# Performance work log

Measured on AMD Instinct MI355X. Metric: run time of the kernel, lower is better.

## Reference

```python
import jax, jax.numpy as jnp
import numpy as np

EPS = 1e-5

def rmsnorm(x, g):
    var = jnp.mean(jnp.square(x), axis=-1, keepdims=True)
    return x * jax.lax.rsqrt(var + EPS) * g

def setup_inputs() -> dict:
    key = jax.random.key(0)
    ks = jax.random.split(key, 8)
    B, S, T, D = 2, 2048, 2048, 1024
    H, HKV, HD = 16, 4, 64
    std = 0.02
    return {
        "x": jax.random.normal(ks[0], (B, S, D), jnp.float32),
        "kv": jax.random.normal(ks[1], (B, T, D), jnp.float32),
        "wq": jax.random.normal(ks[2], (H * HD, D), jnp.float32) * std,
        "wk": jax.random.normal(ks[3], (HKV * HD, D), jnp.float32) * std,
        "wv": jax.random.normal(ks[4], (HKV * HD, D), jnp.float32) * std,
        "wo": jax.random.normal(ks[5], (D, H * HD), jnp.float32) * std,
        "gq": jnp.ones((D,), jnp.float32),
        "gkv": jnp.ones((D,), jnp.float32),
    }

def reference(x, kv, wq, wk, wv, wo, gq, gkv):
    B, S, D = x.shape
    T = kv.shape[1]
    H, HKV, HD = 16, 4, 64
    R = H // HKV  # heads per kv group
    xn = rmsnorm(x, gq)
    kvn = rmsnorm(kv, gkv)
    # projections
    q = (xn @ wq.T).reshape(B, S, HKV, R, HD)   # grouped query heads
    k = (kvn @ wk.T).reshape(B, T, HKV, HD)
    v = (kvn @ wv.T).reshape(B, T, HKV, HD)
    scale = 1.0 / jnp.sqrt(jnp.float32(HD))
    # block-mask is None -> full dense cross attention; GQA via broadcast einsum
    scores = jnp.einsum('bsgrd,btgd->bgrst', q, k) * scale  # [B,HKV,R,S,T]
    probs = jax.nn.softmax(scores, axis=-1)
    out = jnp.einsum('bgrst,btgd->bsgrd', probs, v)  # [B,S,HKV,R,HD]
    out = out.reshape(B, S, H * HD) @ wo.T
    return x + out
```

## Files before the change

kernel.cpp:

```cpp
#include <hip/hip_runtime.h>

#define DEV __device__ __forceinline__

typedef __attribute__((ext_vector_type(8))) _Float16 h8;
typedef __attribute__((ext_vector_type(4))) float f32x4;
typedef __attribute__((ext_vector_type(16))) float f32x16;
typedef __fp16 __attribute__((ext_vector_type(2))) hh2;

DEV unsigned short f2h(float f) {
  union { _Float16 h[2]; unsigned short u[2]; } v;
  v.h[0] = (_Float16)f;
  return v.u[0];
}

DEV float h2f(unsigned short u) {
  union { _Float16 h[2]; unsigned short u[2]; } v;
  v.u[0] = u;
  return (float)v.h[0];
}

DEV void async_load16(const void* g, void* l) {
  __builtin_amdgcn_global_load_lds(
      (const __attribute__((address_space(1))) void*)g,
      (__attribute__((address_space(3))) void*)l,
      16, 0, 0);
}

DEV void pl32swap(unsigned int& a, unsigned int& b) {
  asm("v_permlane32_swap_b32 %0, %1" : "+v"(a), "+v"(b));
}


__global__ __launch_bounds__(256) void prep(const float* __restrict__ x,
                                            const float* __restrict__ kv,
                                            const float* __restrict__ wq,
                                            const float* __restrict__ wk,
                                            const float* __restrict__ wv,
                                            const float* __restrict__ wo,
                                            const float* __restrict__ gq,
                                            const float* __restrict__ gkv,
                                            unsigned short* __restrict__ wqb,
                                            unsigned short* __restrict__ wkvb,
                                            unsigned short* __restrict__ wob,
                                            unsigned short* __restrict__ xn,
                                            unsigned short* __restrict__ kvn,
                                            float qscale) {
  const int b = blockIdx.x, tid = threadIdx.x;
  if (b < 2560) {
    const float* src;
    unsigned short* dst;
    float sc = 1.0f;
    int base;
    if (b < 1024) { src = wq; dst = wqb; sc = qscale; base = b; }
    else if (b < 1280) { src = wk; dst = wkvb; base = b - 1024; }
    else if (b < 1536) { src = wv; dst = wkvb + 262144; base = b - 1280; }
    else { src = wo; dst = wob; base = b - 1536; }
    const int i = (base * 256 + tid) * 4;
    float4 v = *(const float4*)&src[i];
    ushort4 o;
    o.x = f2h(v.x * sc); o.y = f2h(v.y * sc);
    o.z = f2h(v.z * sc); o.w = f2h(v.w * sc);
    *(ushort4*)&dst[i] = o;
    return;
  }
  int row = b - 2560;
  const float* src;
  const float* g;
  unsigned short* dst;
  if (row < 4096) { src = x; g = gq; dst = xn; }
  else { row -= 4096; src = kv; g = gkv; dst = kvn; }
  const float* xr = src + (size_t)row * 1024;
  float4 v = *(const float4*)&xr[tid * 4];
  float ss = v.x * v.x + v.y * v.y + v.z * v.z + v.w * v.w;
  ss += __shfl_xor(ss, 32); ss += __shfl_xor(ss, 16);
  ss += __shfl_xor(ss, 8);  ss += __shfl_xor(ss, 4);
  ss += __shfl_xor(ss, 2);  ss += __shfl_xor(ss, 1);
  __shared__ float red[4];
  if ((tid & 63) == 0) red[tid >> 6] = ss;
  __syncthreads();
  float tot = red[0] + red[1] + red[2] + red[3];
  float inv = rsqrtf(tot * (1.0f / 1024.0f) + 1e-5f);
  float4 gv = *(const float4*)&g[tid * 4];
  ushort4 o;
  o.x = f2h(v.x * inv * gv.x); o.y = f2h(v.y * inv * gv.y);
  o.z = f2h(v.z * inv * gv.z); o.w = f2h(v.w * inv * gv.w);
  *(ushort4*)&dst[(size_t)row * 1024 + tid * 4] = o;
}

__global__ __launch_bounds__(256) void proj_gemm(const unsigned short* __restrict__ xn,
                                                 const unsigned short* __restrict__ kvn,
                                                 const unsigned short* __restrict__ wqb,
                                                 const unsigned short* __restrict__ wkvb,
                                                 unsigned short* __restrict__ qb,
                                                 unsigned short* __restrict__ kb,
                                                 unsigned short* __restrict__ vTb) {
  __shared__ unsigned short Al[2][2][128 * 32];
  __shared__ unsigned short Bl[2][2][64 * 32];
  const int tid = threadIdx.x;
  const int w = tid >> 6, l = tid & 63;
  const int quad = l >> 4, ln = l & 15;
  const int wm0 = (w >> 1) * 64, wn0 = (w & 1) * 32;
  const int r4 = l >> 2;
  const int c4s = (((l & 3) ^ ((l >> 3) & 3))) * 8;
  const int qs8 = (quad ^ ((l >> 1) & 3)) * 8;

  int z = blockIdx.x;
  const unsigned short *A, *W;
  int m0, n0, isq;
  if (z < 512) {
    A = xn; W = wqb; isq = 1;
    m0 = (((z >> 7) << 3) + (z & 7)) * 128;
    n0 = ((z >> 3) & 15) * 64;
  } else {
    z -= 512; A = kvn; W = wkvb; isq = 0;
    m0 = (((z >> 6) << 3) + (z & 7)) * 128;
    n0 = ((z >> 3) & 7) * 64;
  }

  f32x4 acc[4][2] = {};

  auto stage = [&](int buf, int kk) {
#pragma unroll
    for (int j = 0; j < 6; ++j) {
      const int idx = w * 6 + j;
      if (idx < 16) {
        const int p = idx >> 3, rb = (idx & 7) * 16;
        async_load16(A + (size_t)(m0 + rb + r4) * 1024 + kk + p * 32 + c4s,
                     &Al[buf][p][rb * 32]);
      } else {
        const int ib = idx - 16;
        const int p = ib >> 2, rb = (ib & 3) * 16;
        async_load16(W + (size_t)(n0 + rb + r4) * 1024 + kk + p * 32 + c4s,
                     &Bl[buf][p][rb * 32]);
      }
    }
  };

  stage(0, 0);
#pragma unroll 2
  for (int it = 0; it < 16; ++it) {
    const int buf = it & 1;
    __syncthreads();
    if (it < 15) stage(buf ^ 1, (it + 1) * 64);
#pragma unroll
    for (int kc = 0; kc < 2; ++kc) {
      h8 af[4], bf[2];
#pragma unroll
      for (int mi = 0; mi < 4; ++mi)
        af[mi] = *(const h8*)&Al[buf][kc][(wm0 + mi * 16 + ln) * 32 + qs8];
#pragma unroll
      for (int ni = 0; ni < 2; ++ni)
        bf[ni] = *(const h8*)&Bl[buf][kc][(wn0 + ni * 16 + ln) * 32 + qs8];
#pragma unroll
      for (int mi = 0; mi < 4; ++mi)
#pragma unroll
        for (int ni = 0; ni < 2; ++ni)
          acc[mi][ni] = __builtin_amdgcn_mfma_f32_16x16x32_f16(af[mi], bf[ni], acc[mi][ni], 0, 0, 0);
    }
  }

#pragma unroll
  for (int mi = 0; mi < 4; ++mi)
#pragma unroll
    for (int ni = 0; ni < 2; ++ni)
#pragma unroll
      for (int r = 0; r < 4; ++r) {
        const int row = m0 + wm0 + mi * 16 + quad * 4 + r;
        const int col = n0 + wn0 + ni * 16 + ln;
        const unsigned short v = f2h(acc[mi][ni][r]);
        if (isq) {
          qb[((size_t)row << 10) + col] = v;
        } else if (col < 256) {
          kb[(size_t)row * 256 + col] = v;
        } else {
          const int c2 = col - 256, gg = c2 >> 6, dd = c2 & 63;
          const int bb = row >> 11, t = row & 2047;
          vTb[((size_t)((bb * 4 + gg) * 64 + dd) << 11) + t] = v;
        }
      }
}

__global__ __launch_bounds__(256) void o_gemm(const unsigned short* __restrict__ O0,
                                              const unsigned short* __restrict__ O1,
                                              const float* __restrict__ l0p,
                                              const float* __restrict__ l1p,
                                              const unsigned short* __restrict__ wob,
                                              const float* __restrict__ x,
                                              float* __restrict__ out) {
  __shared__ unsigned short Al[2][2][128 * 32];
  __shared__ unsigned short Bl[2][2][64 * 32];
  __shared__ float Linv[16 * 128];
  const int tid = threadIdx.x;
  const int w = tid >> 6, l = tid & 63;
  const int quad = l >> 4, ln = l & 15;
  const int wm0 = (w >> 1) * 64, wn0 = (w & 1) * 32;
  const int r4 = l >> 2;
  const int c4s = (((l & 3) ^ ((l >> 3) & 3))) * 8;
  const int qs8 = (quad ^ ((l >> 1) & 3)) * 8;

  const int z = blockIdx.x;
  const int m0 = (((z >> 7) << 3) + (z & 7)) * 128;
  const int n0 = ((z >> 3) & 15) * 64;

  {
    const int h = tid >> 4, r0 = (tid & 15) * 8;
#pragma unroll
    for (int i = 0; i < 8; ++i) {
      const int r = r0 + i;
      const size_t li = (size_t)(m0 + r) * 16 + h;
      Linv[h * 128 + r] = 1.0f / (l0p[li] + l1p[li]);
    }
  }
  __syncthreads();

  const int srow = tid >> 3;
  const int sp = (tid >> 2) & 1;
  const int ss = tid & 3;

  auto stageA = [&](int buf, int kk) {
    const int h = kk >> 6;
#pragma unroll
    for (int ps = 0; ps < 4; ++ps) {
      const int row = ps * 32 + srow;
      const size_t gidx = (size_t)(m0 + row) * 1024 + kk + sp * 32 + ss * 8;
      h8 a0 = *(const h8*)&O0[gidx];
      h8 a1 = *(const h8*)&O1[gidx];
      const _Float16 lv = (_Float16)Linv[h * 128 + row];
      h8 sum = a0 + a1;
#pragma unroll
      for (int q2 = 0; q2 < 8; ++q2) sum[q2] *= lv;
      const int sl = ss ^ ((row >> 1) & 3);
      *(h8*)&Al[buf][sp][row * 32 + sl * 8] = sum;
    }
  };
  auto stageB = [&](int buf, int kk) {
#pragma unroll
    for (int j = 0; j < 2; ++j) {
      const int ib = w * 2 + j;
      const int p = ib >> 2, rb = (ib & 3) * 16;
      async_load16(wob + (size_t)(n0 + rb + r4) * 1024 + kk + p * 32 + c4s,
                   &Bl[buf][p][rb * 32]);
    }
  };

  f32x4 acc[4][2] = {};
  stageB(0, 0);
  stageA(0, 0);
  for (int it = 0; it < 16; ++it) {
    const int buf = it & 1;
    __syncthreads();
    if (it < 15) { stageB(buf ^ 1, (it + 1) * 64); stageA(buf ^ 1, (it + 1) * 64); }
#pragma unroll
    for (int kc = 0; kc < 2; ++kc) {
      h8 af[4], bf[2];
#pragma unroll
      for (int mi = 0; mi < 4; ++mi)
        af[mi] = *(const h8*)&Al[buf][kc][(wm0 + mi * 16 + ln) * 32 + qs8];
#pragma unroll
      for (int ni = 0; ni < 2; ++ni)
        bf[ni] = *(const h8*)&Bl[buf][kc][(wn0 + ni * 16 + ln) * 32 + qs8];
#pragma unroll
      for (int mi = 0; mi < 4; ++mi)
#pragma unroll
        for (int ni = 0; ni < 2; ++ni)
          acc[mi][ni] = __builtin_amdgcn_mfma_f32_16x16x32_f16(af[mi], bf[ni], acc[mi][ni], 0, 0, 0);
    }
  }

#pragma unroll
  for (int mi = 0; mi < 4; ++mi)
#pragma unroll
    for (int ni = 0; ni < 2; ++ni)
#pragma unroll
      for (int r = 0; r < 4; ++r) {
        const int row = m0 + wm0 + mi * 16 + quad * 4 + r;
        const int col = n0 + wn0 + ni * 16 + ln;
        const size_t idx = ((size_t)row << 10) + col;
        out[idx] = x[idx] + acc[mi][ni][r];
      }
}

__global__ __launch_bounds__(256, 2) void flash_attn(const unsigned short* __restrict__ q,
                                                     const unsigned short* __restrict__ k,
                                                     const unsigned short* __restrict__ vT,
                                                     unsigned short* __restrict__ o0,
                                                     unsigned short* __restrict__ o1,
                                                     float* __restrict__ l0p,
                                                     float* __restrict__ l1p) {
  __shared__ __align__(16) unsigned short Kl[3][64 * 64];
  __shared__ __align__(16) unsigned short Vl[3][64 * 64];

  const int tid = threadIdx.x;
  const int w = tid >> 6, l = tid & 63;
  const int lq = l & 31, hi = l >> 5;
  const int r8 = l >> 3, c8 = l & 7;
  const int csw = (c8 ^ r8) * 8;
  const int rsw = lq & 7;
  const int s0 = blockIdx.x * 256;
  const int h = blockIdx.y, g = h >> 2;
  const int b = blockIdx.z >> 1, ts = blockIdx.z & 1;
  const int tbase = ts << 10;

  unsigned short* Opart = ts ? o1 : o0;
  float* lpart = ts ? l1p : l0p;

  size_t qrow[2];
  qrow[0] = (size_t)(b * 2048 + s0 + w * 64 + lq);
  qrow[1] = qrow[0] + 32;

  h8 qf[2][4];
#pragma unroll
  for (int q2 = 0; q2 < 2; ++q2)
#pragma unroll
    for (int ks = 0; ks < 4; ++ks)
      qf[q2][ks] = *(const h8*)&q[(qrow[q2] << 10) + h * 64 + ks * 16 + hi * 8];
  asm volatile("s_waitcnt vmcnt(0)" ::: "memory");

  int aoff[4];
#pragma unroll
  for (int j = 0; j < 4; ++j)
    aoff[j] = (lq * 64 + (((2 * j + hi) ^ rsw)) * 8) * 2;

  f32x16 oacc[2][2] = {};
  float lsum[2] = {0.0f, 0.0f};

  const unsigned short* kbase = k + ((size_t)(b * 2048)) * 256 + g * 64;
  const unsigned short* vbase = vT + (((size_t)(b * 4 + g) * 64) << 11);

  const hh2 one2 = {(__fp16)1.0f, (__fp16)1.0f};

  auto stage = [&](int sb, int t0) {
#pragma unroll
    for (int j = 0; j < 2; ++j) {
      const int idx = w * 2 + j;
      async_load16(kbase + (size_t)(t0 + idx * 8 + r8) * 256 + csw,
                   &Kl[sb][idx * 512]);
      async_load16(vbase + (((size_t)(idx * 8 + r8)) << 11) + t0 + csw,
                   &Vl[sb][idx * 512]);
    }
  };

#define FA_SYNC(N)                                                   \
  do {                                                               \
    asm volatile("s_waitcnt vmcnt(" #N ")" ::: "memory");            \
    __builtin_amdgcn_s_barrier();                                    \
    __builtin_amdgcn_sched_barrier(0);                               \
  } while (0)

#define FA_HALF(CB, TH)                                                        \
  {                                                                            \
    h8 kf[4];                                                                  \
    _Pragma("unroll")                                                          \
    for (int ks = 0; ks < 4; ++ks)                                             \
      kf[ks] = *(const h8*)((const char*)&Kl[CB][(TH) * 2048] + aoff[ks]);     \
    f32x16 st0 = {}, st1 = {};                                                 \
    __builtin_amdgcn_s_setprio(1);                                             \
    _Pragma("unroll")                                                          \
    for (int ks = 0; ks < 4; ++ks) {                                           \
      st0 = __builtin_amdgcn_mfma_f32_32x32x16_f16(kf[ks], qf[0][ks], st0, 0, 0, 0); \
      st1 = __builtin_amdgcn_mfma_f32_32x32x16_f16(kf[ks], qf[1][ks], st1, 0, 0, 0); \
    }                                                                          \
    __builtin_amdgcn_s_setprio(0);                                             \
    unsigned int w0_[8], w1_[8];                                               \
    _Pragma("unroll")                                                          \
    for (int j = 0; j < 8; ++j) {                                              \
      union { hh2 h2; unsigned int u; } pk0, pk1;                              \
      pk0.h2 = __builtin_amdgcn_cvt_pkrtz(__builtin_amdgcn_exp2f(st0[2 * j]),  \
                                          __builtin_amdgcn_exp2f(st0[2 * j + 1])); \
      pk1.h2 = __builtin_amdgcn_cvt_pkrtz(__builtin_amdgcn_exp2f(st1[2 * j]),  \
                                          __builtin_amdgcn_exp2f(st1[2 * j + 1])); \
      lsum[0] = __builtin_amdgcn_fdot2(pk0.h2, one2, lsum[0], false);          \
      lsum[1] = __builtin_amdgcn_fdot2(pk1.h2, one2, lsum[1], false);          \
      w0_[j] = pk0.u; w1_[j] = pk1.u;                                          \
    }                                                                          \
    h8 pf0[2], pf1[2];                                                         \
    {                                                                          \
      unsigned int a0 = w0_[0], b0 = w0_[2]; pl32swap(a0, b0);                 \
      unsigned int a1 = w0_[1], b1 = w0_[3]; pl32swap(a1, b1);                 \
      unsigned int a4 = w0_[4], b4 = w0_[6]; pl32swap(a4, b4);                 \
      unsigned int a5 = w0_[5], b5 = w0_[7]; pl32swap(a5, b5);                 \
      union { unsigned int u[4]; h8 v; } f0, f1;                               \
      f0.u[0] = a0; f0.u[1] = a1; f0.u[2] = b0; f0.u[3] = b1;                  \
      f1.u[0] = a4; f1.u[1] = a5; f1.u[2] = b4; f1.u[3] = b5;                  \
      pf0[0] = f0.v; pf0[1] = f1.v;                                            \
      unsigned int c0 = w1_[0], d0 = w1_[2]; pl32swap(c0, d0);                 \
      unsigned int c1 = w1_[1], d1 = w1_[3]; pl32swap(c1, d1);                 \
      unsigned int c4 = w1_[4], d4 = w1_[6]; pl32swap(c4, d4);                 \
      unsigned int c5 = w1_[5], d5 = w1_[7]; pl32swap(c5, d5);                 \
      union { unsigned int u[4]; h8 v; } f2, f3;                               \
      f2.u[0] = c0; f2.u[1] = c1; f2.u[2] = d0; f2.u[3] = d1;                  \
      f3.u[0] = c4; f3.u[1] = c5; f3.u[2] = d4; f3.u[3] = d5;                  \
      pf1[0] = f2.v; pf1[1] = f3.v;                                            \
    }                                                                          \
    __builtin_amdgcn_s_setprio(1);                                             \
    _Pragma("unroll")                                                          \
    for (int cc = 0; cc < 2; ++cc) {                                           \
      const int c = (TH) * 2 + cc;                                             \
      h8 v0 = *(const h8*)((const char*)&Vl[CB][0] + aoff[c]);                 \
      h8 v1 = *(const h8*)((const char*)&Vl[CB][2048] + aoff[c]);              \
      oacc[0][0] = __builtin_amdgcn_mfma_f32_32x32x16_f16(v0, pf0[cc], oacc[0][0], 0, 0, 0); \
      oacc[1][0] = __builtin_amdgcn_mfma_f32_32x32x16_f16(v0, pf1[cc], oacc[1][0], 0, 0, 0); \
      oacc[0][1] = __builtin_amdgcn_mfma_f32_32x32x16_f16(v1, pf0[cc], oacc[0][1], 0, 0, 0); \
      oacc[1][1] = __builtin_amdgcn_mfma_f32_32x32x16_f16(v1, pf1[cc], oacc[1][1], 0, 0, 0); \
    }                                                                          \
    __builtin_amdgcn_s_setprio(0);                                             \
  }

#define FA_BODY(CB) { FA_HALF(CB, 0) FA_HALF(CB, 1) }

  stage(0, tbase);
  stage(1, tbase + 64);

  for (int tt = 0; tt < 15; tt += 3) {
    FA_SYNC(4);
    stage(2, tbase + (tt + 2) * 64);
    FA_BODY(0);
    FA_SYNC(4);
    stage(0, tbase + (tt + 3) * 64);
    FA_BODY(1);
    FA_SYNC(4);
    if (tt + 4 < 16) stage(1, tbase + (tt + 4) * 64);
    FA_BODY(2);
  }
  FA_SYNC(0);
  FA_BODY(0);

#undef FA_BODY
#undef FA_HALF
#undef FA_SYNC

#pragma unroll
  for (int q2 = 0; q2 < 2; ++q2) {
    float ls = lsum[q2];
    ls += __shfl_xor(ls, 32);
    if (l < 32) lpart[qrow[q2] * 16 + h] = ls;
#pragma unroll
    for (int dblk = 0; dblk < 2; ++dblk)
#pragma unroll
      for (int qd = 0; qd < 4; ++qd) {
        ushort4 o;
        o.x = f2h(oacc[q2][dblk][qd * 4 + 0]);
        o.y = f2h(oacc[q2][dblk][qd * 4 + 1]);
        o.z = f2h(oacc[q2][dblk][qd * 4 + 2]);
        o.w = f2h(oacc[q2][dblk][qd * 4 + 3]);
        *(ushort4*)&Opart[(qrow[q2] << 10) + h * 64 + dblk * 32 + qd * 8 + hi * 4] = o;
      }
  }
}

extern "C" void kernel_launch(void* const* d_in, const int* in_sizes, int n_in,
                              void* d_out, int out_size, void* d_ws, size_t ws_size,
                              hipStream_t stream) {
  const float* x   = (const float*)d_in[0];
  const float* kv  = (const float*)d_in[1];
  const float* wq  = (const float*)d_in[2];
  const float* wk  = (const float*)d_in[3];
  const float* wv  = (const float*)d_in[4];
  const float* wo  = (const float*)d_in[5];
  const float* gq  = (const float*)d_in[6];
  const float* gkv = (const float*)d_in[7];

  char* ws = (char*)d_ws;
  unsigned short* xn   = (unsigned short*)(ws);
  unsigned short* kvn  = (unsigned short*)(ws + 8388608);
  unsigned short* qb   = (unsigned short*)(ws + 16777216);
  unsigned short* kb   = (unsigned short*)(ws + 25165824);
  unsigned short* vTb  = (unsigned short*)(ws + 27262976);
  unsigned short* wqb  = (unsigned short*)(ws + 37748736);
  unsigned short* wkvb = (unsigned short*)(ws + 39845888);
  unsigned short* wob  = (unsigned short*)(ws + 40894464);
  unsigned short* Opart0 = xn;
  unsigned short* Opart1 = kvn;
  float* l0p = (float*)wqb;
  float* l1p = (float*)(ws + 37748736 + 262144);

  const float qscale = 0.18033688011112042f;

  prep<<<10752, 256, 0, stream>>>(x, kv, wq, wk, wv, wo, gq, gkv,
                                  wqb, wkvb, wob, xn, kvn, qscale);

  proj_gemm<<<768, 256, 0, stream>>>(xn, kvn, wqb, wkvb, qb, kb, vTb);

  flash_attn<<<dim3(8, 16, 4), 256, 0, stream>>>(qb, kb, vTb, Opart0, Opart1, l0p, l1p);

  o_gemm<<<512, 256, 0, stream>>>(Opart0, Opart1, l0p, l1p, wob, x, (float*)d_out);
}
```

Measured before the change: 190.4 us.

## Widen GEMM tiles to 128x128 and batch rows per block in prep

The projection and output GEMMs move from 128x64 to 128x128 block tiles, so each warp now holds a 64x64 accumulator. This doubles operand reuse per LDS load and halves the grid sizes. The prep kernel now processes four weight chunks per block and one RMSNorm row per wavefront, which removes the shared-memory reduction and __syncthreads and cuts the block count by four. The trade-offs are higher register and LDS use and fewer blocks in flight for the GEMMs on a device with many CUs.

```diff
diff --git a/kernel.cpp b/kernel.cpp
--- a/kernel.cpp
+++ b/kernel.cpp
@@ -46,60 +46,68 @@
                                             unsigned short* __restrict__ kvn,
                                             float qscale) {
   const int b = blockIdx.x, tid = threadIdx.x;
-  if (b < 2560) {
+  if (b < 640) {
     const float* src;
     unsigned short* dst;
     float sc = 1.0f;
     int base;
-    if (b < 1024) { src = wq; dst = wqb; sc = qscale; base = b; }
-    else if (b < 1280) { src = wk; dst = wkvb; base = b - 1024; }
-    else if (b < 1536) { src = wv; dst = wkvb + 262144; base = b - 1280; }
-    else { src = wo; dst = wob; base = b - 1536; }
-    const int i = (base * 256 + tid) * 4;
-    float4 v = *(const float4*)&src[i];
-    ushort4 o;
-    o.x = f2h(v.x * sc); o.y = f2h(v.y * sc);
-    o.z = f2h(v.z * sc); o.w = f2h(v.w * sc);
-    *(ushort4*)&dst[i] = o;
+    if (b < 256) { src = wq; dst = wqb; sc = qscale; base = b; }
+    else if (b < 320) { src = wk; dst = wkvb; base = b - 256; }
+    else if (b < 384) { src = wv; dst = wkvb + 262144; base = b - 320; }
+    else { src = wo; dst = wob; base = b - 384; }
+#pragma unroll
+    for (int j = 0; j < 4; ++j) {
+      const int i = base * 4096 + j * 1024 + tid * 4;
+      float4 v = *(const float4*)&src[i];
+      ushort4 o;
+      o.x = f2h(v.x * sc); o.y = f2h(v.y * sc);
+      o.z = f2h(v.z * sc); o.w = f2h(v.w * sc);
+      *(ushort4*)&dst[i] = o;
+    }
     return;
   }
-  int row = b - 2560;
+  const int w = tid >> 6, l = tid & 63;
+  int row = (b - 640) * 4 + w;
   const float* src;
   const float* g;
   unsigned short* dst;
   if (row < 4096) { src = x; g = gq; dst = xn; }
   else { row -= 4096; src = kv; g = gkv; dst = kvn; }
   const float* xr = src + (size_t)row * 1024;
-  float4 v = *(const float4*)&xr[tid * 4];
-  float ss = v.x * v.x + v.y * v.y + v.z * v.z + v.w * v.w;
+  float4 v[4];
+  float ss = 0.0f;
+#pragma unroll
+  for (int i = 0; i < 4; ++i) {
+    v[i] = *(const float4*)&xr[i * 256 + l * 4];
+    ss += v[i].x * v[i].x + v[i].y * v[i].y + v[i].z * v[i].z + v[i].w * v[i].w;
+  }
   ss += __shfl_xor(ss, 32); ss += __shfl_xor(ss, 16);
   ss += __shfl_xor(ss, 8);  ss += __shfl_xor(ss, 4);
   ss += __shfl_xor(ss, 2);  ss += __shfl_xor(ss, 1);
-  __shared__ float red[4];
-  if ((tid & 63) == 0) red[tid >> 6] = ss;
-  __syncthreads();
-  float tot = red[0] + red[1] + red[2] + red[3];
-  float inv = rsqrtf(tot * (1.0f / 1024.0f) + 1e-5f);
-  float4 gv = *(const float4*)&g[tid * 4];
-  ushort4 o;
-  o.x = f2h(v.x * inv * gv.x); o.y = f2h(v.y * inv * gv.y);
-  o.z = f2h(v.z * inv * gv.z); o.w = f2h(v.w * inv * gv.w);
-  *(ushort4*)&dst[(size_t)row * 1024 + tid * 4] = o;
-}
-
-__global__ __launch_bounds__(256) void proj_gemm(const unsigned short* __restrict__ xn,
-                                                 const unsigned short* __restrict__ kvn,
-                                                 const unsigned short* __restrict__ wqb,
-                                                 const unsigned short* __restrict__ wkvb,
-                                                 unsigned short* __restrict__ qb,
-                                                 unsigned short* __restrict__ kb,
-                                                 unsigned short* __restrict__ vTb) {
+  const float inv = rsqrtf(ss * (1.0f / 1024.0f) + 1e-5f);
+#pragma unroll
+  for (int i = 0; i < 4; ++i) {
+    float4 gv = *(const float4*)&g[i * 256 + l * 4];
+    ushort4 o;
+    o.x = f2h(v[i].x * inv * gv.x); o.y = f2h(v[i].y * inv * gv.y);
+    o.z = f2h(v[i].z * inv * gv.z); o.w = f2h(v[i].w * inv * gv.w);
+    *(ushort4*)&dst[(size_t)row * 1024 + i * 256 + l * 4] = o;
+  }
+}
+
+__global__ __launch_bounds__(256, 2) void proj_gemm(const unsigned short* __restrict__ xn,
+                                                    const unsigned short* __restrict__ kvn,
+                                                    const unsigned short* __restrict__ wqb,
+                                                    const unsigned short* __restrict__ wkvb,
+                                                    unsigned short* __restrict__ qb,
+                                                    unsigned short* __restrict__ kb,
+                                                    unsigned short* __restrict__ vTb) {
   __shared__ unsigned short Al[2][2][128 * 32];
-  __shared__ unsigned short Bl[2][2][64 * 32];
+  __shared__ unsigned short Bl[2][2][128 * 32];
   const int tid = threadIdx.x;
   const int w = tid >> 6, l = tid & 63;
   const int quad = l >> 4, ln = l & 15;
-  const int wm0 = (w >> 1) * 64, wn0 = (w & 1) * 32;
+  const int wm0 = (w >> 1) * 64, wn0 = (w & 1) * 64;
   const int r4 = l >> 2;
   const int c4s = (((l & 3) ^ ((l >> 3) & 3))) * 8;
   const int qs8 = (quad ^ ((l >> 1) & 3)) * 8;
@@ -107,29 +115,29 @@
   int z = blockIdx.x;
   const unsigned short *A, *W;
   int m0, n0, isq;
-  if (z < 512) {
+  if (z < 256) {
     A = xn; W = wqb; isq = 1;
-    m0 = (((z >> 7) << 3) + (z & 7)) * 128;
-    n0 = ((z >> 3) & 15) * 64;
+    m0 = (((z >> 6) << 3) + (z & 7)) * 128;
+    n0 = ((z >> 3) & 7) * 128;
   } else {
-    z -= 512; A = kvn; W = wkvb; isq = 0;
-    m0 = (((z >> 6) << 3) + (z & 7)) * 128;
-    n0 = ((z >> 3) & 7) * 64;
-  }
-
-  f32x4 acc[4][2] = {};
+    z -= 256; A = kvn; W = wkvb; isq = 0;
+    m0 = (((z >> 5) << 3) + (z & 7)) * 128;
+    n0 = ((z >> 3) & 3) * 128;
+  }
+
+  f32x4 acc[4][4] = {};
 
   auto stage = [&](int buf, int kk) {
 #pragma unroll
-    for (int j = 0; j < 6; ++j) {
-      const int idx = w * 6 + j;
+    for (int j = 0; j < 8; ++j) {
+      const int idx = w * 8 + j;
       if (idx < 16) {
         const int p = idx >> 3, rb = (idx & 7) * 16;
         async_load16(A + (size_t)(m0 + rb + r4) * 1024 + kk + p * 32 + c4s,
                      &Al[buf][p][rb * 32]);
       } else {
         const int ib = idx - 16;
-        const int p = ib >> 2, rb = (ib & 3) * 16;
+        const int p = ib >> 3, rb = (ib & 7) * 16;
         async_load16(W + (size_t)(n0 + rb + r4) * 1024 + kk + p * 32 + c4s,
                      &Bl[buf][p][rb * 32]);
       }
@@ -137,24 +145,23 @@
   };
 
   stage(0, 0);
-#pragma unroll 2
   for (int it = 0; it < 16; ++it) {
     const int buf = it & 1;
     __syncthreads();
     if (it < 15) stage(buf ^ 1, (it + 1) * 64);
 #pragma unroll
     for (int kc = 0; kc < 2; ++kc) {
-      h8 af[4], bf[2];
+      h8 af[4], bf[4];
 #pragma unroll
       for (int mi = 0; mi < 4; ++mi)
         af[mi] = *(const h8*)&Al[buf][kc][(wm0 + mi * 16 + ln) * 32 + qs8];
 #pragma unroll
-      for (int ni = 0; ni < 2; ++ni)
+      for (int ni = 0; ni < 4; ++ni)
         bf[ni] = *(const h8*)&Bl[buf][kc][(wn0 + ni * 16 + ln) * 32 + qs8];
 #pragma unroll
       for (int mi = 0; mi < 4; ++mi)
 #pragma unroll
-        for (int ni = 0; ni < 2; ++ni)
+        for (int ni = 0; ni < 4; ++ni)
           acc[mi][ni] = __builtin_amdgcn_mfma_f32_16x16x32_f16(af[mi], bf[ni], acc[mi][ni], 0, 0, 0);
     }
   }
@@ -162,7 +169,7 @@
 #pragma unroll
   for (int mi = 0; mi < 4; ++mi)
 #pragma unroll
-    for (int ni = 0; ni < 2; ++ni)
+    for (int ni = 0; ni < 4; ++ni)
 #pragma unroll
       for (int r = 0; r < 4; ++r) {
         const int row = m0 + wm0 + mi * 16 + quad * 4 + r;
@@ -188,19 +195,19 @@
                                               const float* __restrict__ x,
                                               float* __restrict__ out) {
   __shared__ unsigned short Al[2][2][128 * 32];
-  __shared__ unsigned short Bl[2][2][64 * 32];
+  __shared__ unsigned short Bl[2][2][128 * 32];
   __shared__ float Linv[16 * 128];
   const int tid = threadIdx.x;
   const int w = tid >> 6, l = tid & 63;
   const int quad = l >> 4, ln = l & 15;
-  const int wm0 = (w >> 1) * 64, wn0 = (w & 1) * 32;
+  const int wm0 = (w >> 1) * 64, wn0 = (w & 1) * 64;
   const int r4 = l >> 2;
   const int c4s = (((l & 3) ^ ((l >> 3) & 3))) * 8;
   const int qs8 = (quad ^ ((l >> 1) & 3)) * 8;
 
   const int z = blockIdx.x;
-  const int m0 = (((z >> 7) << 3) + (z & 7)) * 128;
-  const int n0 = ((z >> 3) & 15) * 64;
+  const int m0 = (((z >> 6) << 3) + (z & 7)) * 128;
+  const int n0 = ((z >> 3) & 7) * 128;
 
   {
     const int h = tid >> 4, r0 = (tid & 15) * 8;
@@ -235,15 +242,15 @@
   };
   auto stageB = [&](int buf, int kk) {
 #pragma unroll
-    for (int j = 0; j < 2; ++j) {
-      const int ib = w * 2 + j;
-      const int p = ib >> 2, rb = (ib & 3) * 16;
+    for (int j = 0; j < 4; ++j) {
+      const int ib = w * 4 + j;
+      const int p = ib >> 3, rb = (ib & 7) * 16;
       async_load16(wob + (size_t)(n0 + rb + r4) * 1024 + kk + p * 32 + c4s,
                    &Bl[buf][p][rb * 32]);
     }
   };
 
-  f32x4 acc[4][2] = {};
+  f32x4 acc[4][4] = {};
   stageB(0, 0);
   stageA(0, 0);
   for (int it = 0; it < 16; ++it) {
@@ -252,17 +259,17 @@
     if (it < 15) { stageB(buf ^ 1, (it + 1) * 64); stageA(buf ^ 1, (it + 1) * 64); }
 #pragma unroll
     for (int kc = 0; kc < 2; ++kc) {
-      h8 af[4], bf[2];
+      h8 af[4], bf[4];
 #pragma unroll
       for (int mi = 0; mi < 4; ++mi)
         af[mi] = *(const h8*)&Al[buf][kc][(wm0 + mi * 16 + ln) * 32 + qs8];
 #pragma unroll
-      for (int ni = 0; ni < 2; ++ni)
+      for (int ni = 0; ni < 4; ++ni)
         bf[ni] = *(const h8*)&Bl[buf][kc][(wn0 + ni * 16 + ln) * 32 + qs8];
 #pragma unroll
       for (int mi = 0; mi < 4; ++mi)
 #pragma unroll
-        for (int ni = 0; ni < 2; ++ni)
+        for (int ni = 0; ni < 4; ++ni)
           acc[mi][ni] = __builtin_amdgcn_mfma_f32_16x16x32_f16(af[mi], bf[ni], acc[mi][ni], 0, 0, 0);
     }
   }
@@ -270,7 +277,7 @@
 #pragma unroll
   for (int mi = 0; mi < 4; ++mi)
 #pragma unroll
-    for (int ni = 0; ni < 2; ++ni)
+    for (int ni = 0; ni < 4; ++ni)
 #pragma unroll
       for (int r = 0; r < 4; ++r) {
         const int row = m0 + wm0 + mi * 16 + quad * 4 + r;
@@ -476,12 +483,12 @@
 
   const float qscale = 0.18033688011112042f;
 
-  prep<<<10752, 256, 0, stream>>>(x, kv, wq, wk, wv, wo, gq, gkv,
-                                  wqb, wkvb, wob, xn, kvn, qscale);
-
-  proj_gemm<<<768, 256, 0, stream>>>(xn, kvn, wqb, wkvb, qb, kb, vTb);
+  prep<<<2688, 256, 0, stream>>>(x, kv, wq, wk, wv, wo, gq, gkv,
+                                 wqb, wkvb, wob, xn, kvn, qscale);
+
+  proj_gemm<<<384, 256, 0, stream>>>(xn, kvn, wqb, wkvb, qb, kb, vTb);
 
   flash_attn<<<dim3(8, 16, 4), 256, 0, stream>>>(qb, kb, vTb, Opart0, Opart1, l0p, l1p);
 
-  o_gemm<<<512, 256, 0, stream>>>(Opart0, Opart1, l0p, l1p, wob, x, (float*)d_out);
-}
+  o_gemm<<<256, 256, 0, stream>>>(Opart0, Opart1, l0p, l1p, wob, x, (float*)d_out);
+}
```

Result: no change. 190.2 us (-0.1%).
